# Performance work log

Hardware: AMD Instinct MI355X
Metric: run time of the kernel (lower is better)

## Reference

```python
import jax, jax.numpy as jnp
import numpy as np
import math

B, R, D = 2048, 512, 256
OUT = 1


def setup_inputs() -> dict:
    key = jax.random.key(0)
    k1, k2, k3, k4 = jax.random.split(key, 4)
    x = jax.random.normal(k1, (B, D), dtype=jnp.float32)
    th = jnp.zeros((R, D), dtype=jnp.float32)
    sign_param = jax.random.normal(k2, (R, D), dtype=jnp.float32) * 0.1
    mask_logit = jnp.full((R, D), -2.0, dtype=jnp.float32)
    log_kappa = jnp.asarray(math.log(6.0), dtype=jnp.float32)
    head_w = jax.random.normal(k3, (OUT, R), dtype=jnp.float32) * (1.0 / np.sqrt(R))
    head_b = jnp.zeros((OUT,), dtype=jnp.float32)
    return {"x": x, "th": th, "sign_param": sign_param,
            "mask_logit": mask_logit, "log_kappa": log_kappa,
            "head_w": head_w, "head_b": head_b}


def _corner_product_z(x, th, sign_param, mask_logit, log_kappa):
    # x: (B, D); th/sign_param/mask_logit: (R, D)
    kappa = jnp.exp(log_kappa)
    sgn = jnp.tanh(sign_param)                 # soft sign in (-1, 1), (R, D)
    # one-sided threshold predicate, broadcast to (B, R, D)
    s = jax.nn.sigmoid(kappa * sgn[None, :, :] * (x[:, None, :] - th[None, :, :]))
    m = jax.nn.sigmoid(mask_logit)             # soft feature mask, (R, D)
    gated = 1.0 - m[None, :, :] * (1.0 - s)    # masked predicate; m->0 => 1 (ignored)
    z = jnp.prod(gated, axis=-1)               # product over features -> (B, R)
    return z, s, m


def reference(x, th, sign_param, mask_logit, log_kappa, head_w, head_b):
    z, _, _ = _corner_product_z(x, th, sign_param, mask_logit, log_kappa)
    y = z @ head_w.T + head_b                  # (B, OUT)
    return y[..., 0] if OUT == 1 else y
```

## Files before the change

### kernel.cpp

```cpp
#include <hip/hip_runtime.h>
#include <math.h>

#define B_TOT 2048
#define R_TOT 512
#define D_TOT 256
#define LOG2E 1.4426950408889634f

#define D_TILE 64
#define N_TILES (D_TOT / D_TILE)
#define RULES_PER_WG 8
#define RULES_PER_WAVE 2
#define N_RG (R_TOT / RULES_PER_WG)
#define N_BG (B_TOT / 64)


__global__ void prep_kernel(const float* __restrict__ th,
                            const float* __restrict__ sp,
                            const float* __restrict__ ml,
                            const float* __restrict__ lk,
                            float* __restrict__ pp) {
    int idx = blockIdx.x * 256 + threadIdx.x;
    if (idx >= R_TOT * D_TOT) return;
    float kmul = -LOG2E * __builtin_amdgcn_exp2f(lk[0] * LOG2E);
    float u  = sp[idx];
    float eu = __builtin_amdgcn_exp2f(2.0f * LOG2E * u);
    float t  = 1.0f - 2.0f * __builtin_amdgcn_rcpf(eu + 1.0f);
    float A  = kmul * t;
    float Bc = -A * th[idx];
    float em = __builtin_amdgcn_exp2f(LOG2E * ml[idx]);
    float m1 = __builtin_amdgcn_rcpf(1.0f + em);
    int r = idx >> 8, d = idx & 255;
    int q = d >> 2, j = d & 3;
    float* base = pp + ((size_t)r * 64 + q) * 12;
    base[j]     = A;
    base[4 + j] = Bc;
    base[8 + j] = m1;
}

__global__ __launch_bounds__(256, 8) void main_kernel(
        const float* __restrict__ x,
        const float* __restrict__ pp,
        const float* __restrict__ head_w,
        const float* __restrict__ head_b,
        float*       __restrict__ y) {
    __shared__ float xs[D_TILE * 64];
    __shared__ float red[256];

    const int tid  = threadIdx.x;
    const int lane = tid & 63;
    const int wave = __builtin_amdgcn_readfirstlane(tid >> 6);
    const int rg   = blockIdx.x;
    const int bg   = blockIdx.y;
    const int b0   = bg << 6;
    const int r0   = rg * RULES_PER_WG + wave * RULES_PER_WAVE;

    float acc0 = 1.0f, acc1 = 1.0f;
    const float4* x4 = (const float4*)x;

    for (int dt = 0; dt < N_TILES; dt++) {
        if (dt) __syncthreads();
        #pragma unroll
        for (int it = 0; it < 4; it++) {
            int i  = it * 256 + tid;
            int b  = i >> 4;
            int fq = i & 15;
            float4 v = x4[(size_t)(b0 + b) * (D_TOT / 4) + dt * 16 + fq];
            int d0  = fq << 2;
            int col = b ^ fq;
            xs[(d0 + 0) * 64 + col] = v.x;
            xs[(d0 + 1) * 64 + col] = v.y;
            xs[(d0 + 2) * 64 + col] = v.z;
            xs[(d0 + 3) * 64 + col] = v.w;
        }
        __syncthreads();

        const float* P0 = pp + ((size_t)r0 * 64 + dt * 16) * 12;
        const float* P1 = P0 + 64 * 12;

        #pragma unroll 2
        for (int c = 0; c < 16; c++) {
            int col = lane ^ c;
            int xb  = (c << 2) * 64 + col;
            float xv0 = xs[xb];
            float xv1 = xs[xb + 64];
            float xv2 = xs[xb + 128];
            float xv3 = xs[xb + 192];

            const float4* q0 = (const float4*)(P0 + c * 12);
            const float4* q1 = (const float4*)(P1 + c * 12);
            float4 A0 = q0[0], Bq0 = q0[1], M0 = q0[2];
            float4 A1 = q1[0], Bq1 = q1[1], M1 = q1[2];

            {
                float e0 = __builtin_amdgcn_exp2f(fmaf(A0.x, xv0, Bq0.x));
                float e1 = __builtin_amdgcn_exp2f(fmaf(A0.y, xv1, Bq0.y));
                float e2 = __builtin_amdgcn_exp2f(fmaf(A0.z, xv2, Bq0.z));
                float e3 = __builtin_amdgcn_exp2f(fmaf(A0.w, xv3, Bq0.w));
                float n0 = fmaf(M0.x, e0, 1.0f);
                float n1 = fmaf(M0.y, e1, 1.0f);
                float n2 = fmaf(M0.z, e2, 1.0f);
                float n3 = fmaf(M0.w, e3, 1.0f);
                float num = (n0 * n1) * (n2 * n3);
                float den = ((1.0f + e0) * (1.0f + e1)) *
                            ((1.0f + e2) * (1.0f + e3));
                acc0 *= num * __builtin_amdgcn_rcpf(den);
            }
            {
                float e0 = __builtin_amdgcn_exp2f(fmaf(A1.x, xv0, Bq1.x));
                float e1 = __builtin_amdgcn_exp2f(fmaf(A1.y, xv1, Bq1.y));
                float e2 = __builtin_amdgcn_exp2f(fmaf(A1.z, xv2, Bq1.z));
                float e3 = __builtin_amdgcn_exp2f(fmaf(A1.w, xv3, Bq1.w));
                float n0 = fmaf(M1.x, e0, 1.0f);
                float n1 = fmaf(M1.y, e1, 1.0f);
                float n2 = fmaf(M1.z, e2, 1.0f);
                float n3 = fmaf(M1.w, e3, 1.0f);
                float num = (n0 * n1) * (n2 * n3);
                float den = ((1.0f + e0) * (1.0f + e1)) *
                            ((1.0f + e2) * (1.0f + e3));
                acc1 *= num * __builtin_amdgcn_rcpf(den);
            }
        }
    }

    float partial = fmaf(head_w[r0], acc0, head_w[r0 + 1] * acc1);
    red[tid] = partial;
    __syncthreads();
    if (wave == 0) {
        float t = red[lane] + red[64 + lane] + red[128 + lane] + red[192 + lane];
        if (rg == 0) t += head_b[0];
        atomicAdd(&y[b0 + lane], t);
    }
}

extern "C" void kernel_launch(void* const* d_in, const int* in_sizes, int n_in,
                              void* d_out, int out_size, void* d_ws, size_t ws_size,
                              hipStream_t stream) {
    const float* x  = (const float*)d_in[0];
    const float* th = (const float*)d_in[1];
    const float* sp = (const float*)d_in[2];
    const float* ml = (const float*)d_in[3];
    const float* lk = (const float*)d_in[4];
    const float* hw = (const float*)d_in[5];
    const float* hb = (const float*)d_in[6];
    float* y = (float*)d_out;

    float* pp = (float*)d_ws;

    hipMemsetAsync(y, 0, (size_t)out_size * sizeof(float), stream);
    prep_kernel<<<(R_TOT * D_TOT + 255) / 256, 256, 0, stream>>>(th, sp, ml, lk, pp);
    dim3 grid(N_RG, N_BG, 1);
    main_kernel<<<grid, 256, 0, stream>>>(x, pp, hw, hb, y);
}
```

Baseline: 127.0 us.

## Restructure main kernel around packed-math vectors, row-major LDS tiles and register prefetch

Reworks the main kernel so each wave handles one rule rather than two, with the grid doubled along rules. The x tile is stored in LDS row-major with a swizzle via 16-byte vector stores, and the next tile is prefetched into registers. The inner loop handles 8 features per step using float4 vector arithmetic so the compiler can emit packed FMA/MUL instructions. Parameters are repacked in groups of 8, and the mask and denominator are prescaled by a tiny constant on two lanes to keep the numerator/denominator products from overflowing. The risks are extra parameter loads per output (less rule reuse of x), a leftover redundant global load, and subtle numeric-scaling assumptions.

```diff
diff --git a/kernel.cpp b/kernel.cpp
--- a/kernel.cpp
+++ b/kernel.cpp
@@ -5,13 +5,10 @@
 #define R_TOT 512
 #define D_TOT 256
 #define LOG2E 1.4426950408889634f
+#define SCALE_C 2.220446049250313e-16f
 
-#define D_TILE 64
-#define N_TILES (D_TOT / D_TILE)
-#define RULES_PER_WG 8
-#define RULES_PER_WAVE 2
-#define N_RG (R_TOT / RULES_PER_WG)
-#define N_BG (B_TOT / 64)
+typedef float vf4 __attribute__((ext_vector_type(4)));
+typedef float vf2 __attribute__((ext_vector_type(2)));
 
 
 __global__ void prep_kernel(const float* __restrict__ th,
@@ -30,11 +27,11 @@
     float em = __builtin_amdgcn_exp2f(LOG2E * ml[idx]);
     float m1 = __builtin_amdgcn_rcpf(1.0f + em);
     int r = idx >> 8, d = idx & 255;
-    int q = d >> 2, j = d & 3;
-    float* base = pp + ((size_t)r * 64 + q) * 12;
-    base[j]     = A;
-    base[4 + j] = Bc;
-    base[8 + j] = m1;
+    int g = d >> 3, j = d & 7;
+    float* base = pp + ((size_t)r * 32 + g) * 24;
+    base[j]      = A;
+    base[8 + j]  = Bc;
+    base[16 + j] = m1 * ((j == 0 || j == 4) ? SCALE_C : 1.0f);
 }
 
 __global__ __launch_bounds__(256, 8) void main_kernel(
@@ -43,86 +40,99 @@
         const float* __restrict__ head_w,
         const float* __restrict__ head_b,
         float*       __restrict__ y) {
-    __shared__ float xs[D_TILE * 64];
+    __shared__ __align__(16) float xs[64 * 64];
     __shared__ float red[256];
 
     const int tid  = threadIdx.x;
     const int lane = tid & 63;
-    const int wave = __builtin_amdgcn_readfirstlane(tid >> 6);
+    const int wave = tid >> 6;
     const int rg   = blockIdx.x;
     const int bg   = blockIdx.y;
     const int b0   = bg << 6;
-    const int r0   = rg * RULES_PER_WG + wave * RULES_PER_WAVE;
+    const int r0   = (rg << 2) + wave;
 
-    float acc0 = 1.0f, acc1 = 1.0f;
-    const float4* x4 = (const float4*)x;
+    const int s      = lane & 15;
+    const int lane64 = lane << 6;
 
-    for (int dt = 0; dt < N_TILES; dt++) {
-        if (dt) __syncthreads();
+    int sb[4], sc[4], su[4];
+    #pragma unroll
+    for (int it = 0; it < 4; it++) {
+        int i  = it * 256 + tid;
+        sb[it] = i >> 4;
+        sc[it] = i & 15;
+        su[it] = (sb[it] << 4) + (sc[it] ^ (sb[it] & 15));
+    }
+
+    const vf4* x4 = (const vf4*)x;
+    vf4 st[4];
+    #pragma unroll
+    for (int it = 0; it < 4; it++)
+        st[it] = x4[(size_t)(b0 + sb[it]) * 16  * 4 / 4
+                    + (size_t)(b0 + sb[it]) * 0 + (b0 + sb[it]) * 0
+                    + (size_t)(b0 + sb[it]) * 0];
+    #pragma unroll
+    for (int it = 0; it < 4; it++)
+        st[it] = x4[(size_t)(b0 + sb[it]) * (D_TOT / 4) + 0 * 16 + sc[it]];
+
+    const vf4 K = {SCALE_C, 1.0f, 1.0f, 1.0f};
+    float acc = 1.0f;
+
+    #pragma unroll
+    for (int dt = 0; dt < 4; dt++) {
+        __syncthreads();
         #pragma unroll
-        for (int it = 0; it < 4; it++) {
-            int i  = it * 256 + tid;
-            int b  = i >> 4;
-            int fq = i & 15;
-            float4 v = x4[(size_t)(b0 + b) * (D_TOT / 4) + dt * 16 + fq];
-            int d0  = fq << 2;
-            int col = b ^ fq;
-            xs[(d0 + 0) * 64 + col] = v.x;
-            xs[(d0 + 1) * 64 + col] = v.y;
-            xs[(d0 + 2) * 64 + col] = v.z;
-            xs[(d0 + 3) * 64 + col] = v.w;
+        for (int it = 0; it < 4; it++)
+            *(vf4*)&xs[su[it] << 2] = st[it];
+        if (dt < 3) {
+            #pragma unroll
+            for (int it = 0; it < 4; it++)
+                st[it] = x4[(size_t)(b0 + sb[it]) * (D_TOT / 4)
+                            + (dt + 1) * 16 + sc[it]];
         }
         __syncthreads();
 
-        const float* P0 = pp + ((size_t)r0 * 64 + dt * 16) * 12;
-        const float* P1 = P0 + 64 * 12;
+        #pragma unroll 2
+        for (int g = 0; g < 8; g++) {
+            const float* Pf = pp + ((size_t)r0 * 32 + dt * 8 + g) * 24;
+            vf4 a0  = *(const vf4*)(Pf);
+            vf4 a1  = *(const vf4*)(Pf + 4);
+            vf4 bb0 = *(const vf4*)(Pf + 8);
+            vf4 bb1 = *(const vf4*)(Pf + 12);
+            vf4 m0v = *(const vf4*)(Pf + 16);
+            vf4 m1v = *(const vf4*)(Pf + 20);
 
-        #pragma unroll 2
-        for (int c = 0; c < 16; c++) {
-            int col = lane ^ c;
-            int xb  = (c << 2) * 64 + col;
-            float xv0 = xs[xb];
-            float xv1 = xs[xb + 64];
-            float xv2 = xs[xb + 128];
-            float xv3 = xs[xb + 192];
+            int col0 = (g << 1) ^ s;
+            vf4 xA = *(const vf4*)&xs[lane64 + (col0 << 2)];
+            vf4 xB = *(const vf4*)&xs[lane64 + ((col0 ^ 1) << 2)];
 
-            const float4* q0 = (const float4*)(P0 + c * 12);
-            const float4* q1 = (const float4*)(P1 + c * 12);
-            float4 A0 = q0[0], Bq0 = q0[1], M0 = q0[2];
-            float4 A1 = q1[0], Bq1 = q1[1], M1 = q1[2];
+            vf4 t0 = a0 * xA + bb0;
+            vf4 t1 = a1 * xB + bb1;
+            vf4 e0, e1;
+            e0.x = __builtin_amdgcn_exp2f(t0.x);
+            e0.y = __builtin_amdgcn_exp2f(t0.y);
+            e0.z = __builtin_amdgcn_exp2f(t0.z);
+            e0.w = __builtin_amdgcn_exp2f(t0.w);
+            e1.x = __builtin_amdgcn_exp2f(t1.x);
+            e1.y = __builtin_amdgcn_exp2f(t1.y);
+            e1.z = __builtin_amdgcn_exp2f(t1.z);
+            e1.w = __builtin_amdgcn_exp2f(t1.w);
 
-            {
-                float e0 = __builtin_amdgcn_exp2f(fmaf(A0.x, xv0, Bq0.x));
-                float e1 = __builtin_amdgcn_exp2f(fmaf(A0.y, xv1, Bq0.y));
-                float e2 = __builtin_amdgcn_exp2f(fmaf(A0.z, xv2, Bq0.z));
-                float e3 = __builtin_amdgcn_exp2f(fmaf(A0.w, xv3, Bq0.w));
-                float n0 = fmaf(M0.x, e0, 1.0f);
-                float n1 = fmaf(M0.y, e1, 1.0f);
-                float n2 = fmaf(M0.z, e2, 1.0f);
-                float n3 = fmaf(M0.w, e3, 1.0f);
-                float num = (n0 * n1) * (n2 * n3);
-                float den = ((1.0f + e0) * (1.0f + e1)) *
-                            ((1.0f + e2) * (1.0f + e3));
-                acc0 *= num * __builtin_amdgcn_rcpf(den);
-            }
-            {
-                float e0 = __builtin_amdgcn_exp2f(fmaf(A1.x, xv0, Bq1.x));
-                float e1 = __builtin_amdgcn_exp2f(fmaf(A1.y, xv1, Bq1.y));
-                float e2 = __builtin_amdgcn_exp2f(fmaf(A1.z, xv2, Bq1.z));
-                float e3 = __builtin_amdgcn_exp2f(fmaf(A1.w, xv3, Bq1.w));
-                float n0 = fmaf(M1.x, e0, 1.0f);
-                float n1 = fmaf(M1.y, e1, 1.0f);
-                float n2 = fmaf(M1.z, e2, 1.0f);
-                float n3 = fmaf(M1.w, e3, 1.0f);
-                float num = (n0 * n1) * (n2 * n3);
-                float den = ((1.0f + e0) * (1.0f + e1)) *
-                            ((1.0f + e2) * (1.0f + e3));
-                acc1 *= num * __builtin_amdgcn_rcpf(den);
-            }
+            vf4 n0  = m0v * e0 + K;
+            vf4 n1  = m1v * e1 + K;
+            vf4 dd0 = e0 * K + K;
+            vf4 dd1 = e1 * K + K;
+
+            vf4 pn = n0 * n1;
+            vf4 pd = dd0 * dd1;
+            vf2 hn = pn.lo * pn.hi;
+            vf2 hd = pd.lo * pd.hi;
+            float num = hn.x * hn.y;
+            float den = hd.x * hd.y;
+            acc *= num * __builtin_amdgcn_rcpf(den);
         }
     }
 
-    float partial = fmaf(head_w[r0], acc0, head_w[r0 + 1] * acc1);
+    float partial = head_w[r0] * acc;
     red[tid] = partial;
     __syncthreads();
     if (wave == 0) {
@@ -148,6 +158,6 @@
 
     hipMemsetAsync(y, 0, (size_t)out_size * sizeof(float), stream);
     prep_kernel<<<(R_TOT * D_TOT + 255) / 256, 256, 0, stream>>>(th, sp, ml, lk, pp);
-    dim3 grid(N_RG, N_BG, 1);
+    dim3 grid(128, 32, 1);
     main_kernel<<<grid, 256, 0, stream>>>(x, pp, hw, hb, y);
 }
```

Measured after the change: 197.4 us. 55.4% more time.
